# Kernel optimization log

Measured on AMD Instinct MI355X. Metric: run time of the kernel, lower is better.

Reference implementation:

```python
import jax, jax.numpy as jnp
import numpy as np

B, S, D, H = 2, 2048, 1024, 16
HD = D // H  # 64


def setup_inputs() -> dict:
    key = jax.random.key(0)
    ks = jax.random.split(key, 10)
    s = 1.0 / np.sqrt(D)
    X = jax.random.normal(ks[0], (B, S, D), dtype=jnp.float32)
    # pad the last 256 key positions (nonzero = ignore); causal rows still
    # attend to earlier unpadded keys so no all-masked rows.
    kpm = jnp.broadcast_to((jnp.arange(S) >= S - 256).astype(jnp.int32), (B, S))
    return {
        "X": X,
        "key_padding_mask": kpm,
        "Wq": jax.random.uniform(ks[1], (D, D), jnp.float32, -s, s),
        "bq": jax.random.uniform(ks[2], (D,), jnp.float32, -s, s),
        "Wk": jax.random.uniform(ks[3], (D, D), jnp.float32, -s, s),
        "bk": jax.random.uniform(ks[4], (D,), jnp.float32, -s, s),
        "Wv": jax.random.uniform(ks[5], (D, D), jnp.float32, -s, s),
        "bv": jax.random.uniform(ks[6], (D,), jnp.float32, -s, s),
        "Wo": jax.random.uniform(ks[7], (D, D), jnp.float32, -s, s),
        "bo": jax.random.uniform(ks[8], (D,), jnp.float32, -s, s),
    }


def _mha(X, kpm, Wq, bq, Wk, bk, Wv, bv, Wo, bo):
    b, s, d = X.shape
    def heads(t):  # (b,s,d) -> (b,H,s,hd)
        return t.reshape(b, s, H, HD).transpose(0, 2, 1, 3)
    Q = heads(X @ Wq.T + bq)
    K = heads(X @ Wk.T + bk)
    V = heads(X @ Wv.T + bv)
    scores = jnp.einsum('bhqd,bhkd->bhqk', Q, K) / jnp.sqrt(jnp.float32(HD))
    causal = jnp.triu(jnp.ones((s, s), dtype=bool), k=1)  # True above diag
    scores = jnp.where(causal[None, None], -jnp.inf, scores)
    scores = jnp.where(kpm[:, None, None, :] != 0, -jnp.inf, scores)
    A = jax.nn.softmax(scores, axis=-1)
    out = jnp.einsum('bhqk,bhkd->bhqd', A, V)  # (b,H,s,hd)
    out = out.transpose(0, 2, 1, 3).reshape(b, s, d)
    return out @ Wo.T + bo


def reference(X, key_padding_mask, Wq, bq, Wk, bk, Wv, bv, Wo, bo):
    return _mha(X, key_padding_mask, Wq, bq, Wk, bk, Wv, bv, Wo, bo)
```

## Files before the change

### kernel.cpp

```cpp
#include <hip/hip_runtime.h>
#include <math.h>

#define DEV __device__ __forceinline__

typedef __attribute__((ext_vector_type(4))) float f32x4;
typedef __attribute__((ext_vector_type(8))) __bf16 bf16x8;

static constexpr int Bc = 2, Sc = 2048, Dc = 1024, Hc = 16, HDc = 64;
static constexpr int LDQ = 3 * Dc;
static constexpr float SCL = 0.125f * 1.44269504f;

DEV unsigned short f2b(float f) {
  union { float f; unsigned int u; } c; c.f = f;
  unsigned int u = c.u;
  unsigned int r = (u + 0x7fffu + ((u >> 16) & 1u)) >> 16;
  return (unsigned short)r;
}

DEV void async16(const void* g, void* l) {
  __builtin_amdgcn_global_load_lds(
      (__attribute__((address_space(1))) void*)(void*)g,
      (__attribute__((address_space(3))) void*)l, 16, 0, 0);
}

DEV int swz(int r, int c) { return r * 64 + (c ^ ((r & 7) << 3)); }

__global__ void cvt_x(const float* __restrict__ in,
                      unsigned short* __restrict__ out, int n4) {
  int i = blockIdx.x * blockDim.x + threadIdx.x;
  if (i < n4) {
    const float4 v = reinterpret_cast<const float4*>(in)[i];
    ushort4 o;
    o.x = f2b(v.x); o.y = f2b(v.y); o.z = f2b(v.z); o.w = f2b(v.w);
    reinterpret_cast<ushort4*>(out)[i] = o;
  }
}

__global__ void cvt_w(const float* __restrict__ w0, const float* __restrict__ w1,
                      const float* __restrict__ w2, const float* __restrict__ w3,
                      unsigned short* __restrict__ out) {
  const float* src = blockIdx.y == 0 ? w0
                     : blockIdx.y == 1 ? w1
                     : blockIdx.y == 2 ? w2 : w3;
  const int i = blockIdx.x * blockDim.x + threadIdx.x;
  const float4 v = reinterpret_cast<const float4*>(src)[i];
  ushort4 o;
  o.x = f2b(v.x); o.y = f2b(v.y); o.z = f2b(v.z); o.w = f2b(v.w);
  reinterpret_cast<ushort4*>(out)[(size_t)blockIdx.y * (Dc * Dc / 4) + i] = o;
}

template <typename OUT>
__global__ __launch_bounds__(256, 2) void gemm_bt(
    const unsigned short* __restrict__ A, const unsigned short* __restrict__ Bm,
    const float* __restrict__ b0, const float* __restrict__ b1,
    const float* __restrict__ b2, OUT* __restrict__ C, int M, int K, int ldc) {
  __shared__ unsigned short As[128 * 64];
  __shared__ unsigned short Bs[128 * 64];
  const int tid = threadIdx.x;
  const int wave = tid >> 6, lane = tid & 63;
  const int wr = wave >> 1, wc = wave & 1;
  const int row0 = blockIdx.x * 128, col0 = blockIdx.y * 128;
  const int srow = lane >> 3, scol = (lane & 7) * 8;

  f32x4 acc[4][4];
#pragma unroll
  for (int m = 0; m < 4; ++m)
#pragma unroll
    for (int n = 0; n < 4; ++n) acc[m][n] = {0.f, 0.f, 0.f, 0.f};

  for (int k0 = 0; k0 < K; k0 += 64) {
    __syncthreads();
#pragma unroll
    for (int c = 0; c < 4; ++c) {
      const int rr = (wave * 4 + c) * 8 + srow;
      async16(A + (size_t)(row0 + rr) * K + k0 + scol,
              (char*)As + (wave * 4 + c) * 1024);
      async16(Bm + (size_t)(col0 + rr) * K + k0 + scol,
              (char*)Bs + (wave * 4 + c) * 1024);
    }
    __syncthreads();
#pragma unroll
    for (int ks = 0; ks < 2; ++ks) {
      const int kk = ks * 32 + (lane >> 4) * 8;
      bf16x8 af[4], bfr[4];
#pragma unroll
      for (int m = 0; m < 4; ++m)
        af[m] = *reinterpret_cast<const bf16x8*>(
            &As[(wr * 64 + m * 16 + (lane & 15)) * 64 + kk]);
#pragma unroll
      for (int n = 0; n < 4; ++n)
        bfr[n] = *reinterpret_cast<const bf16x8*>(
            &Bs[(wc * 64 + n * 16 + (lane & 15)) * 64 + kk]);
#pragma unroll
      for (int m = 0; m < 4; ++m)
#pragma unroll
        for (int n = 0; n < 4; ++n)
          acc[m][n] = __builtin_amdgcn_mfma_f32_16x16x32_bf16(af[m], bfr[n],
                                                              acc[m][n], 0, 0, 0);
    }
  }
  const int r4 = (lane >> 4) * 4, cl = lane & 15;
#pragma unroll
  for (int n = 0; n < 4; ++n) {
    const int gc = col0 + wc * 64 + n * 16 + cl;
    const float* bp = gc < Dc ? b0 : (gc < 2 * Dc ? b1 : b2);
    const float bv = bp[gc & (Dc - 1)];
#pragma unroll
    for (int m = 0; m < 4; ++m) {
#pragma unroll
      for (int j = 0; j < 4; ++j) {
        const int gr = row0 + wr * 64 + m * 16 + r4 + j;
        const float v = acc[m][n][j] + bv;
        if constexpr (sizeof(OUT) == 4)
          C[(size_t)gr * ldc + gc] = v;
        else
          C[(size_t)gr * ldc + gc] = (OUT)f2b(v);
      }
    }
  }
}

__global__ __launch_bounds__(256, 4) void attn_fwd(
    const __bf16* __restrict__ Qg, const __bf16* __restrict__ Kg,
    const __bf16* __restrict__ Vg, const int* __restrict__ kpm,
    __bf16* __restrict__ Og) {
  __shared__ __bf16 QP[64 * 64];
  __shared__ __bf16 Ks[2][64 * 64];
  __shared__ __bf16 Vt[2][64 * 64];

  const int qb = (gridDim.x - 1) - blockIdx.x;
  const int bh = blockIdx.y;
  const int b = bh >> 4, h = bh & 15;
  const int q0 = qb * 64;
  const int tid = threadIdx.x, wave = tid >> 6, lane = tid & 63;
  const size_t base = (size_t)b * Sc * LDQ + (size_t)h * HDc;
  const int srow = lane >> 3;
  const int scol = 8 * ((lane & 7) ^ srow);
  const int hi = lane >> 4, cl = lane & 15, r4 = hi * 4;

  const int vk2 = (tid & 31) * 2, vd8 = (tid >> 5) * 8;
  const __bf16* vbase = Vg + base + (size_t)vk2 * LDQ + vd8;
  const int* mbase = kpm + b * Sc;

  union VV { uint4 q; unsigned short u[8]; };

#pragma unroll
  for (int c = 0; c < 2; ++c) {
    const int rr = (wave * 2 + c) * 8 + srow;
    async16(Qg + base + (size_t)(q0 + rr) * LDQ + scol,
            (char*)QP + (wave * 2 + c) * 1024);
    async16(Kg + base + (size_t)rr * LDQ + scol,
            (char*)Ks[0] + (wave * 2 + c) * 1024);
  }
  VV v0, v1;
  v0.q = *reinterpret_cast<const uint4*>(vbase);
  v1.q = *reinterpret_cast<const uint4*>(vbase + LDQ);
  int mki[4];
#pragma unroll
  for (int n = 0; n < 4; ++n) mki[n] = mbase[n * 16 + cl];
  {
    unsigned int* V32 = reinterpret_cast<unsigned int*>(Vt[0]);
#pragma unroll
    for (int i = 0; i < 8; ++i) {
      const int row = vd8 + i;
      V32[row * 32 + ((tid & 31) ^ ((row & 7) << 2))] =
          (unsigned int)v0.u[i] | ((unsigned int)v1.u[i] << 16);
    }
  }
  __syncthreads();

  bf16x8 qf[2];
#pragma unroll
  for (int ks = 0; ks < 2; ++ks)
    qf[ks] = *reinterpret_cast<const bf16x8*>(
        &QP[swz(wave * 16 + cl, ks * 32 + hi * 8)]);
  __bf16* Ps = QP + wave * 1024;

  bf16x8 ones;
#pragma unroll
  for (int i = 0; i < 8; ++i) ones[i] = (__bf16)1.0f;

  f32x4 o[4], lacc;
  float m_[4];
#pragma unroll
  for (int n = 0; n < 4; ++n) o[n] = {0.f, 0.f, 0.f, 0.f};
  lacc = {0.f, 0.f, 0.f, 0.f};
#pragma unroll
  for (int j = 0; j < 4; ++j) m_[j] = -1e30f;

  int pb = 0;
  for (int kb = 0; kb <= qb; ++kb) {
    const bool diag = (kb == qb);
    VV n0, n1;
    int nmk[4];
    if (!diag) {
      const int k1 = (kb + 1) * 64;
#pragma unroll
      for (int c = 0; c < 2; ++c) {
        const int rr = (wave * 2 + c) * 8 + srow;
        async16(Kg + base + (size_t)(k1 + rr) * LDQ + scol,
                (char*)Ks[pb ^ 1] + (wave * 2 + c) * 1024);
      }
      n0.q = *reinterpret_cast<const uint4*>(vbase + (size_t)k1 * LDQ);
      n1.q = *reinterpret_cast<const uint4*>(vbase + (size_t)(k1 + 1) * LDQ);
#pragma unroll
      for (int n = 0; n < 4; ++n) nmk[n] = mbase[k1 + n * 16 + cl];
    }

    f32x4 sa[4];
#pragma unroll
    for (int n = 0; n < 4; ++n) sa[n] = {0.f, 0.f, 0.f, 0.f};
#pragma unroll
    for (int ks = 0; ks < 2; ++ks) {
      const int kk = ks * 32 + hi * 8;
#pragma unroll
      for (int n = 0; n < 4; ++n) {
        if (!(diag && n > wave)) {
          const bf16x8 kf = *reinterpret_cast<const bf16x8*>(
              &Ks[pb][swz(n * 16 + cl, kk)]);
          sa[n] = __builtin_amdgcn_mfma_f32_16x16x32_bf16(qf[ks], kf, sa[n],
                                                          0, 0, 0);
        }
      }
    }
    float pm[4] = {-1e30f, -1e30f, -1e30f, -1e30f};
#pragma unroll
    for (int n = 0; n < 4; ++n) {
      const float mf = mki[n] ? -1e30f : 0.0f;
#pragma unroll
      for (int j = 0; j < 4; ++j) {
        float s2 = fmaf(sa[n][j], SCL, mf);
        if (diag && (n * 16 + cl > wave * 16 + r4 + j)) s2 = -1e30f;
        sa[n][j] = s2;
        pm[j] = fmaxf(pm[j], s2);
      }
    }
    const bool ok = (pm[0] - m_[0] <= 8.f) && (pm[1] - m_[1] <= 8.f) &&
                    (pm[2] - m_[2] <= 8.f) && (pm[3] - m_[3] <= 8.f);
    if (!__all(ok)) {
#pragma unroll
      for (int off = 1; off < 16; off <<= 1)
#pragma unroll
        for (int j = 0; j < 4; ++j)
          pm[j] = fmaxf(pm[j], __shfl_xor(pm[j], off, 64));
#pragma unroll
      for (int j = 0; j < 4; ++j) {
        const float mn = fmaxf(m_[j], pm[j]);
        const float sc = __builtin_amdgcn_exp2f(m_[j] - mn);
        m_[j] = mn;
        lacc[j] *= sc;
#pragma unroll
        for (int n = 0; n < 4; ++n) o[n][j] *= sc;
      }
    }
#pragma unroll
    for (int n = 0; n < 4; ++n)
#pragma unroll
      for (int j = 0; j < 4; ++j) {
        const float p = __builtin_amdgcn_exp2f(sa[n][j] - m_[j]);
        Ps[swz(r4 + j, n * 16 + cl)] = (__bf16)p;
      }
#pragma unroll
    for (int ks = 0; ks < 2; ++ks) {
      const int kk = ks * 32 + hi * 8;
      const bf16x8 pf = *reinterpret_cast<const bf16x8*>(&Ps[swz(cl, kk)]);
#pragma unroll
      for (int n = 0; n < 4; ++n) {
        const bf16x8 vf = *reinterpret_cast<const bf16x8*>(
            &Vt[pb][swz(n * 16 + cl, kk)]);
        o[n] = __builtin_amdgcn_mfma_f32_16x16x32_bf16(pf, vf, o[n], 0, 0, 0);
      }
      lacc = __builtin_amdgcn_mfma_f32_16x16x32_bf16(pf, ones, lacc, 0, 0, 0);
    }
    if (!diag) {
      unsigned int* V32 = reinterpret_cast<unsigned int*>(Vt[pb ^ 1]);
#pragma unroll
      for (int i = 0; i < 8; ++i) {
        const int row = vd8 + i;
        V32[row * 32 + ((tid & 31) ^ ((row & 7) << 2))] =
            (unsigned int)n0.u[i] | ((unsigned int)n1.u[i] << 16);
      }
#pragma unroll
      for (int n = 0; n < 4; ++n) mki[n] = nmk[n];
    }
    __syncthreads();
    pb ^= 1;
  }

#pragma unroll
  for (int j = 0; j < 4; ++j) {
    const float inv = 1.f / lacc[j];
#pragma unroll
    for (int n = 0; n < 4; ++n)
      Og[(size_t)(b * Sc + q0 + wave * 16 + r4 + j) * Dc + h * HDc + n * 16 +
         cl] = (__bf16)(o[n][j] * inv);
  }
}

extern "C" void kernel_launch(void* const* d_in, const int* in_sizes, int n_in,
                              void* d_out, int out_size, void* d_ws,
                              size_t ws_size, hipStream_t stream) {
  const float* X = (const float*)d_in[0];
  const int* kpm = (const int*)d_in[1];
  const float* Wq = (const float*)d_in[2];
  const float* bq = (const float*)d_in[3];
  const float* Wk = (const float*)d_in[4];
  const float* bk = (const float*)d_in[5];
  const float* Wv = (const float*)d_in[6];
  const float* bv = (const float*)d_in[7];
  const float* Wo = (const float*)d_in[8];
  const float* bo = (const float*)d_in[9];
  float* out = (float*)d_out;

  char* w = (char*)d_ws;
  unsigned short* Xb = (unsigned short*)(w);
  unsigned short* Wqkvb = (unsigned short*)(w + (8u << 20));
  unsigned short* Wob = (unsigned short*)(w + (14u << 20));
  unsigned short* QKVb = (unsigned short*)(w + (16u << 20));
  unsigned short* Ab = (unsigned short*)(w + (40u << 20));

  const int MD = Bc * Sc;
  cvt_x<<<dim3(MD * Dc / 1024), 256, 0, stream>>>(X, Xb, MD * Dc / 4);
  cvt_w<<<dim3(Dc * Dc / 1024, 4), 256, 0, stream>>>(Wq, Wk, Wv, Wo, Wqkvb);

  gemm_bt<unsigned short><<<dim3(MD / 128, LDQ / 128), 256, 0, stream>>>(
      Xb, Wqkvb, bq, bk, bv, QKVb, MD, Dc, LDQ);

  attn_fwd<<<dim3(Sc / 64, Bc * Hc), 256, 0, stream>>>(
      (const __bf16*)QKVb, (const __bf16*)QKVb + Dc,
      (const __bf16*)QKVb + 2 * Dc, kpm, (__bf16*)Ab);

  gemm_bt<float><<<dim3(MD / 128, Dc / 128), 256, 0, stream>>>(
      Ab, Wob, bo, bo, bo, out, MD, Dc, Dc);
}
```

Measured before the change: 142.7 us.

## Pair complementary causal query blocks per workgroup to balance load and share K/V

Each workgroup now processes two query blocks, qb and 31-qb, streaming K/V tiles once and applying them to both, so every workgroup does the same amount of causal work and K/V loads are shared. The grid is halved to 16 blocks in x, which gives 512 workgroups in total. The change also adds s_setprio around the MFMA sections. In exchange it doubles the accumulator registers per thread, which risks lower occupancy, and it adds extra syncs when loading Q.

```diff
diff --git a/kernel.cpp b/kernel.cpp
--- a/kernel.cpp
+++ b/kernel.cpp
@@ -128,15 +128,17 @@
   __shared__ __bf16 Ks[2][64 * 64];
   __shared__ __bf16 Vt[2][64 * 64];
 
-  const int qb = (gridDim.x - 1) - blockIdx.x;
+  const int qbA = blockIdx.x;
+  const int qbB = 31 - qbA;
+  const int q0A = qbA * 64, q0B = qbB * 64;
   const int bh = blockIdx.y;
   const int b = bh >> 4, h = bh & 15;
-  const int q0 = qb * 64;
   const int tid = threadIdx.x, wave = tid >> 6, lane = tid & 63;
   const size_t base = (size_t)b * Sc * LDQ + (size_t)h * HDc;
   const int srow = lane >> 3;
   const int scol = 8 * ((lane & 7) ^ srow);
   const int hi = lane >> 4, cl = lane & 15, r4 = hi * 4;
+  const int gq0A = q0A + wave * 16 + r4, gq0B = q0B + wave * 16 + r4;
 
   const int vk2 = (tid & 31) * 2, vd8 = (tid >> 5) * 8;
   const __bf16* vbase = Vg + base + (size_t)vk2 * LDQ + vd8;
@@ -144,11 +146,52 @@
 
   union VV { uint4 q; unsigned short u[8]; };
 
+  bf16x8 qfA[2], qfB[2];
 #pragma unroll
   for (int c = 0; c < 2; ++c) {
     const int rr = (wave * 2 + c) * 8 + srow;
-    async16(Qg + base + (size_t)(q0 + rr) * LDQ + scol,
+    async16(Qg + base + (size_t)(q0A + rr) * LDQ + scol,
             (char*)QP + (wave * 2 + c) * 1024);
+  }
+  __syncthreads();
+#pragma unroll
+  for (int ks = 0; ks < 2; ++ks)
+    qfA[ks] = *reinterpret_cast<const bf16x8*>(
+        &QP[swz(wave * 16 + cl, ks * 32 + hi * 8)]);
+  __syncthreads();
+#pragma unroll
+  for (int c = 0; c < 2; ++c) {
+    const int rr = (wave * 2 + c) * 8 + srow;
+    async16(Qg + base + (size_t)(q0B + rr) * LDQ + scol,
+            (char*)QP + (wave * 2 + c) * 1024);
+  }
+  __syncthreads();
+#pragma unroll
+  for (int ks = 0; ks < 2; ++ks)
+    qfB[ks] = *reinterpret_cast<const bf16x8*>(
+        &QP[swz(wave * 16 + cl, ks * 32 + hi * 8)]);
+
+  __bf16* Ps = QP + wave * 1024;
+
+  bf16x8 ones;
+#pragma unroll
+  for (int i = 0; i < 8; ++i) ones[i] = (__bf16)1.0f;
+
+  f32x4 oA[4], oB[4], lA, lB;
+  float mA[4], mB[4];
+#pragma unroll
+  for (int n = 0; n < 4; ++n) {
+    oA[n] = {0.f, 0.f, 0.f, 0.f};
+    oB[n] = {0.f, 0.f, 0.f, 0.f};
+  }
+  lA = {0.f, 0.f, 0.f, 0.f};
+  lB = {0.f, 0.f, 0.f, 0.f};
+#pragma unroll
+  for (int j = 0; j < 4; ++j) { mA[j] = -1e30f; mB[j] = -1e30f; }
+
+#pragma unroll
+  for (int c = 0; c < 2; ++c) {
+    const int rr = (wave * 2 + c) * 8 + srow;
     async16(Kg + base + (size_t)rr * LDQ + scol,
             (char*)Ks[0] + (wave * 2 + c) * 1024);
   }
@@ -169,32 +212,14 @@
   }
   __syncthreads();
 
-  bf16x8 qf[2];
-#pragma unroll
-  for (int ks = 0; ks < 2; ++ks)
-    qf[ks] = *reinterpret_cast<const bf16x8*>(
-        &QP[swz(wave * 16 + cl, ks * 32 + hi * 8)]);
-  __bf16* Ps = QP + wave * 1024;
-
-  bf16x8 ones;
-#pragma unroll
-  for (int i = 0; i < 8; ++i) ones[i] = (__bf16)1.0f;
-
-  f32x4 o[4], lacc;
-  float m_[4];
-#pragma unroll
-  for (int n = 0; n < 4; ++n) o[n] = {0.f, 0.f, 0.f, 0.f};
-  lacc = {0.f, 0.f, 0.f, 0.f};
-#pragma unroll
-  for (int j = 0; j < 4; ++j) m_[j] = -1e30f;
-
   int pb = 0;
-  for (int kb = 0; kb <= qb; ++kb) {
-    const bool diag = (kb == qb);
+  for (int kb = 0; kb <= qbB; ++kb) {
+    const bool last = (kb == qbB);
+    const int k0 = kb * 64;
     VV n0, n1;
     int nmk[4];
-    if (!diag) {
-      const int k1 = (kb + 1) * 64;
+    if (!last) {
+      const int k1 = k0 + 64;
 #pragma unroll
       for (int c = 0; c < 2; ++c) {
         const int rr = (wave * 2 + c) * 8 + srow;
@@ -207,72 +232,83 @@
       for (int n = 0; n < 4; ++n) nmk[n] = mbase[k1 + n * 16 + cl];
     }
 
-    f32x4 sa[4];
-#pragma unroll
-    for (int n = 0; n < 4; ++n) sa[n] = {0.f, 0.f, 0.f, 0.f};
-#pragma unroll
-    for (int ks = 0; ks < 2; ++ks) {
-      const int kk = ks * 32 + hi * 8;
+    auto compute = [&](const bf16x8 (&qf)[2], f32x4 (&o)[4], float (&m_)[4],
+                       f32x4& lacc, bool diag, int gq0) {
+      f32x4 sa[4];
+#pragma unroll
+      for (int n = 0; n < 4; ++n) sa[n] = {0.f, 0.f, 0.f, 0.f};
+      __builtin_amdgcn_s_setprio(1);
+#pragma unroll
+      for (int ks = 0; ks < 2; ++ks) {
+        const int kk = ks * 32 + hi * 8;
+#pragma unroll
+        for (int n = 0; n < 4; ++n) {
+          if (!(diag && n > wave)) {
+            const bf16x8 kf = *reinterpret_cast<const bf16x8*>(
+                &Ks[pb][swz(n * 16 + cl, kk)]);
+            sa[n] = __builtin_amdgcn_mfma_f32_16x16x32_bf16(qf[ks], kf, sa[n],
+                                                            0, 0, 0);
+          }
+        }
+      }
+      __builtin_amdgcn_s_setprio(0);
+      float pm[4] = {-1e30f, -1e30f, -1e30f, -1e30f};
 #pragma unroll
       for (int n = 0; n < 4; ++n) {
-        if (!(diag && n > wave)) {
-          const bf16x8 kf = *reinterpret_cast<const bf16x8*>(
-              &Ks[pb][swz(n * 16 + cl, kk)]);
-          sa[n] = __builtin_amdgcn_mfma_f32_16x16x32_bf16(qf[ks], kf, sa[n],
-                                                          0, 0, 0);
-        }
-      }
-    }
-    float pm[4] = {-1e30f, -1e30f, -1e30f, -1e30f};
-#pragma unroll
-    for (int n = 0; n < 4; ++n) {
-      const float mf = mki[n] ? -1e30f : 0.0f;
-#pragma unroll
-      for (int j = 0; j < 4; ++j) {
-        float s2 = fmaf(sa[n][j], SCL, mf);
-        if (diag && (n * 16 + cl > wave * 16 + r4 + j)) s2 = -1e30f;
-        sa[n][j] = s2;
-        pm[j] = fmaxf(pm[j], s2);
-      }
-    }
-    const bool ok = (pm[0] - m_[0] <= 8.f) && (pm[1] - m_[1] <= 8.f) &&
-                    (pm[2] - m_[2] <= 8.f) && (pm[3] - m_[3] <= 8.f);
-    if (!__all(ok)) {
-#pragma unroll
-      for (int off = 1; off < 16; off <<= 1)
-#pragma unroll
-        for (int j = 0; j < 4; ++j)
-          pm[j] = fmaxf(pm[j], __shfl_xor(pm[j], off, 64));
-#pragma unroll
-      for (int j = 0; j < 4; ++j) {
-        const float mn = fmaxf(m_[j], pm[j]);
-        const float sc = __builtin_amdgcn_exp2f(m_[j] - mn);
-        m_[j] = mn;
-        lacc[j] *= sc;
-#pragma unroll
-        for (int n = 0; n < 4; ++n) o[n][j] *= sc;
-      }
-    }
-#pragma unroll
-    for (int n = 0; n < 4; ++n)
-#pragma unroll
-      for (int j = 0; j < 4; ++j) {
-        const float p = __builtin_amdgcn_exp2f(sa[n][j] - m_[j]);
-        Ps[swz(r4 + j, n * 16 + cl)] = (__bf16)p;
-      }
-#pragma unroll
-    for (int ks = 0; ks < 2; ++ks) {
-      const int kk = ks * 32 + hi * 8;
-      const bf16x8 pf = *reinterpret_cast<const bf16x8*>(&Ps[swz(cl, kk)]);
-#pragma unroll
-      for (int n = 0; n < 4; ++n) {
-        const bf16x8 vf = *reinterpret_cast<const bf16x8*>(
-            &Vt[pb][swz(n * 16 + cl, kk)]);
-        o[n] = __builtin_amdgcn_mfma_f32_16x16x32_bf16(pf, vf, o[n], 0, 0, 0);
-      }
-      lacc = __builtin_amdgcn_mfma_f32_16x16x32_bf16(pf, ones, lacc, 0, 0, 0);
-    }
-    if (!diag) {
+        const float mf = mki[n] ? -1e30f : 0.0f;
+#pragma unroll
+        for (int j = 0; j < 4; ++j) {
+          float s2 = fmaf(sa[n][j], SCL, mf);
+          if (diag && (k0 + n * 16 + cl > gq0 + j)) s2 = -1e30f;
+          sa[n][j] = s2;
+          pm[j] = fmaxf(pm[j], s2);
+        }
+      }
+      const bool ok = (pm[0] - m_[0] <= 8.f) && (pm[1] - m_[1] <= 8.f) &&
+                      (pm[2] - m_[2] <= 8.f) && (pm[3] - m_[3] <= 8.f);
+      if (!__all(ok)) {
+#pragma unroll
+        for (int off = 1; off < 16; off <<= 1)
+#pragma unroll
+          for (int j = 0; j < 4; ++j)
+            pm[j] = fmaxf(pm[j], __shfl_xor(pm[j], off, 64));
+#pragma unroll
+        for (int j = 0; j < 4; ++j) {
+          const float mn = fmaxf(m_[j], pm[j]);
+          const float sc = __builtin_amdgcn_exp2f(m_[j] - mn);
+          m_[j] = mn;
+          lacc[j] *= sc;
+#pragma unroll
+          for (int n = 0; n < 4; ++n) o[n][j] *= sc;
+        }
+      }
+#pragma unroll
+      for (int n = 0; n < 4; ++n)
+#pragma unroll
+        for (int j = 0; j < 4; ++j) {
+          const float p = __builtin_amdgcn_exp2f(sa[n][j] - m_[j]);
+          Ps[swz(r4 + j, n * 16 + cl)] = (__bf16)p;
+        }
+      __builtin_amdgcn_s_setprio(1);
+#pragma unroll
+      for (int ks = 0; ks < 2; ++ks) {
+        const int kk = ks * 32 + hi * 8;
+        const bf16x8 pf = *reinterpret_cast<const bf16x8*>(&Ps[swz(cl, kk)]);
+#pragma unroll
+        for (int n = 0; n < 4; ++n) {
+          const bf16x8 vf = *reinterpret_cast<const bf16x8*>(
+              &Vt[pb][swz(n * 16 + cl, kk)]);
+          o[n] = __builtin_amdgcn_mfma_f32_16x16x32_bf16(pf, vf, o[n], 0, 0, 0);
+        }
+        lacc = __builtin_amdgcn_mfma_f32_16x16x32_bf16(pf, ones, lacc, 0, 0, 0);
+      }
+      __builtin_amdgcn_s_setprio(0);
+    };
+
+    if (kb <= qbA) compute(qfA, oA, mA, lA, kb == qbA, gq0A);
+    compute(qfB, oB, mB, lB, last, gq0B);
+
+    if (!last) {
       unsigned int* V32 = reinterpret_cast<unsigned int*>(Vt[pb ^ 1]);
 #pragma unroll
       for (int i = 0; i < 8; ++i) {
@@ -289,11 +325,15 @@
 
 #pragma unroll
   for (int j = 0; j < 4; ++j) {
-    const float inv = 1.f / lacc[j];
-#pragma unroll
-    for (int n = 0; n < 4; ++n)
-      Og[(size_t)(b * Sc + q0 + wave * 16 + r4 + j) * Dc + h * HDc + n * 16 +
-         cl] = (__bf16)(o[n][j] * inv);
+    const float invA = 1.f / lA[j];
+    const float invB = 1.f / lB[j];
+#pragma unroll
+    for (int n = 0; n < 4; ++n) {
+      Og[(size_t)(b * Sc + q0A + wave * 16 + r4 + j) * Dc + h * HDc + n * 16 +
+         cl] = (__bf16)(oA[n][j] * invA);
+      Og[(size_t)(b * Sc + q0B + wave * 16 + r4 + j) * Dc + h * HDc + n * 16 +
+         cl] = (__bf16)(oB[n][j] * invB);
+    }
   }
 }
 
@@ -326,7 +366,7 @@
   gemm_bt<unsigned short><<<dim3(MD / 128, LDQ / 128), 256, 0, stream>>>(
       Xb, Wqkvb, bq, bk, bv, QKVb, MD, Dc, LDQ);
 
-  attn_fwd<<<dim3(Sc / 64, Bc * Hc), 256, 0, stream>>>(
+  attn_fwd<<<dim3(16, Bc * Hc), 256, 0, stream>>>(
       (const __bf16*)QKVb, (const __bf16*)QKVb + Dc,
       (const __bf16*)QKVb + 2 * Dc, kpm, (__bf16*)Ab);
 
```

Measured after the change: 247.1 us. +73.2%, slower.
